# Optimization experiments

Hardware: AMD Instinct MI355X
Metric: run time of the kernel (lower is better)

Reference implementation:

```python
import jax, jax.numpy as jnp
import numpy as np

D_MODEL = 1024
N_HEADS = 16
D_HEAD = 64
D_REC = N_HEADS * D_HEAD  # 1024
BATCH = 4
SEQ = 8192
CHUNK = 64


def _make_decay_bias():
    n_fast, n_medium, n_slow = 5, 6, 5
    b = np.zeros(D_REC, dtype=np.float32)
    fast_end = n_fast * D_HEAD
    medium_end = (n_fast + n_medium) * D_HEAD
    b[:fast_end] = -2.2
    b[fast_end:medium_end] = 0.0
    b[medium_end:] = 4.6
    return jnp.asarray(b)


def setup_inputs() -> dict:
    key = jax.random.key(0)
    k_x, k_w1, k_w2 = jax.random.split(key, 3)
    x = jax.random.normal(k_x, (BATCH, SEQ, D_MODEL), dtype=jnp.float32)
    # nn.Linear(d_model, 3*d_rec, bias=False); stored as [in, out] for clean matmul
    W_aiv = jax.random.normal(k_w1, (D_MODEL, 3 * D_REC), dtype=jnp.float32) / np.sqrt(D_MODEL)
    decay_bias = _make_decay_bias()
    W_mix = jax.random.normal(k_w2, (D_REC, D_MODEL), dtype=jnp.float32) / np.sqrt(D_REC)
    b_mix = jnp.zeros((D_MODEL,), dtype=jnp.float32)
    return {"x": x, "W_aiv": W_aiv, "decay_bias": decay_bias, "W_mix": W_mix, "b_mix": b_mix}


def _chunked_scan(decay, value, chunk_size=CHUNK):
    # decay, value: [b, s, d] float32; gated linear recurrence h_t = a_t*h_{t-1} + u_t
    b, s, d = decay.shape
    pad = (-s) % chunk_size
    if pad:
        decay = jnp.pad(decay, ((0, 0), (0, pad), (0, 0)), constant_values=1.0)
        value = jnp.pad(value, ((0, 0), (0, pad), (0, 0)))
    total = s + pad
    n = total // chunk_size
    dc = decay.reshape(b, n, chunk_size, d)
    vc = value.reshape(b, n, chunk_size, d)
    # intra-chunk: cumulative decay products in log space
    cum_log = jnp.cumsum(jnp.log(jnp.maximum(dc, 1e-10)), axis=2)
    cum_decay = jnp.exp(cum_log)
    weighted = vc / jnp.maximum(cum_decay, 1e-10)
    intra_state = cum_decay * jnp.cumsum(weighted, axis=2)
    # cross-chunk propagation
    chunk_final_state = intra_state[:, :, -1, :]   # [b, n, d]
    chunk_total_decay = cum_decay[:, :, -1, :]     # [b, n, d]
    cum_log_chunk = jnp.cumsum(jnp.log(jnp.maximum(chunk_total_decay, 1e-10)), axis=1)
    cum_chunk_decay = jnp.exp(cum_log_chunk)
    cum_weighted_chunk = jnp.cumsum(chunk_final_state / jnp.maximum(cum_chunk_decay, 1e-10), axis=1)
    zeros = jnp.zeros((b, 1, d), dtype=cum_weighted_chunk.dtype)
    ones = jnp.ones((b, 1, d), dtype=cum_chunk_decay.dtype)
    incoming_cum_weighted = jnp.concatenate([zeros, cum_weighted_chunk[:, :-1]], axis=1)
    incoming_cum_decay = jnp.concatenate([ones, cum_chunk_decay[:, :-1]], axis=1)
    incoming_state = incoming_cum_decay * incoming_cum_weighted  # [b, n, d]
    cross_contrib = cum_decay * incoming_state[:, :, None, :]
    states = (intra_state + cross_contrib).reshape(b, total, d)[:, :s]
    return states


def reference(x, W_aiv, decay_bias, W_mix, b_mix):
    aiv = x @ W_aiv  # [b, s, 3*d_rec]
    a_proj, i_proj, v = jnp.split(aiv, 3, axis=-1)
    a = jax.nn.sigmoid(a_proj + decay_bias)
    i = jax.nn.sigmoid(i_proj)
    input_signal = jnp.sqrt(jnp.maximum(1.0 - a * a, 1e-8)) * (i * v)
    h = _chunked_scan(a.astype(jnp.float32), input_signal.astype(jnp.float32))
    h = h.astype(x.dtype)
    return h @ W_mix + b_mix
```

## Files before the change

### kernel.cpp

```cpp
#include <hip/hip_runtime.h>
#include <cstdint>
#include <cstddef>

#define BATCH   4
#define SEQ     8192
#define DREC    1024
#define CHUNK   64
#define NCHUNK  128
#define M_TOT   (BATCH*SEQ)
#define N_AIV   3072

#define BM 256
#define BN 256
#define BK 32
#define NBUF 4

typedef _Float16 half8 __attribute__((ext_vector_type(8)));
typedef _Float16 half4 __attribute__((ext_vector_type(4)));
typedef float   floatx4 __attribute__((ext_vector_type(4)));

#define LOG2E   1.4426950408889634f
#define NLOG2EPS 33.219281f


__device__ __forceinline__ void gl_lds16(const void* g, void* l) {
    __builtin_amdgcn_global_load_lds(
        (const __attribute__((address_space(1))) void*)g,
        (__attribute__((address_space(3))) void*)l, 16, 0, 0);
}

__device__ __forceinline__ float fast_sigmoid(float z) {
    float e = __builtin_amdgcn_exp2f(-LOG2E * z);
    return __builtin_amdgcn_rcpf(1.f + e);
}

template <bool F16_OUT, bool TWO_PHASE>
__global__ __launch_bounds__(512, 2) void gemm_ff(
    const _Float16* __restrict__ A, int lda,
    const _Float16* __restrict__ BT, int ldb,
    void* __restrict__ Cv, int ldc, int K,
    const float* __restrict__ bias)
{
    __shared__ __align__(16) _Float16 sm[NBUF * 16384];

    const int tid  = threadIdx.x;
    const int lane = tid & 63;
    const int wave = tid >> 6;

    const int nwg = gridDim.x * gridDim.y;
    int lin = blockIdx.y * gridDim.x + blockIdx.x;
    {
        const int cpx = nwg >> 3;
        lin = (lin & 7) * cpx + (lin >> 3);
    }
    const int bx = lin % gridDim.x;
    const int by = lin / gridDim.x;
    const int bm = by * BM;
    const int bn = bx * BN;
    const int wm = (wave >> 2) * 128;
    const int wn = (wave & 3) * 64;

    floatx4 acc[8][4];
    const floatx4 z4 = {0.f, 0.f, 0.f, 0.f};
    #pragma unroll
    for (int i = 0; i < 8; ++i)
        #pragma unroll
        for (int j = 0; j < 4; ++j) acc[i][j] = z4;

    const int o0 = tid * 16, o1 = o0 + 8192;
    const int r0 = o0 >> 6, s0 = (o0 >> 4) & 3;
    const int r1 = o1 >> 6, s1 = (o1 >> 4) & 3;
    const int g0 = (s0 ^ ((r0 >> 1) & 3)) * 8;
    const int g1 = (s1 ^ ((r1 >> 1) & 3)) * 8;
    const size_t aRow0 = (size_t)(bm + r0) * lda;
    const size_t aRow1 = (size_t)(bm + r1) * lda;
    const size_t bRow0 = (size_t)(bn + r0) * ldb;
    const size_t bRow1 = (size_t)(bn + r1) * ldb;

    auto stageA = [&](int t) {
        const int k0 = t * BK;
        char* base = (char*)sm + (t & (NBUF - 1)) * 32768;
        gl_lds16(A + aRow0 + k0 + g0, base + o0);
        gl_lds16(A + aRow1 + k0 + g1, base + o1);
    };
    auto stageB = [&](int t) {
        const int k0 = t * BK;
        char* base = (char*)sm + (t & (NBUF - 1)) * 32768;
        gl_lds16(BT + bRow0 + k0 + g0, base + 16384 + o0);
        gl_lds16(BT + bRow1 + k0 + g1, base + 16384 + o1);
    };

    const int fm = lane & 15;
    const int fq = lane >> 4;
    const int m0 = wm + fm;
    const int n0 = wn + fm;
    const int aoff0 = m0 * BK + ((fq ^ ((m0 >> 1) & 3)) << 3);
    const int boff0 = n0 * BK + ((fq ^ ((n0 >> 1) & 3)) << 3);

    const int NT = K / BK;
    stageA(0); stageB(0);
    if (NT > 1) { stageA(1); stageB(1); }
    if (NT > 2) { stageA(2); stageB(2); }

    for (int t = 0; t < NT; ++t) {
        const int rem = NT - 1 - t;
        if (rem >= 2)      asm volatile("s_waitcnt vmcnt(8)" ::: "memory");
        else if (rem == 1) asm volatile("s_waitcnt vmcnt(4)" ::: "memory");
        else               asm volatile("s_waitcnt vmcnt(0)" ::: "memory");
        __builtin_amdgcn_s_barrier();
        __builtin_amdgcn_sched_barrier(0);

        const _Float16* sA = sm + (t & (NBUF - 1)) * 16384;
        const _Float16* sB = sA + 8192;

        if constexpr (!TWO_PHASE) {
            if (t + 3 < NT) { stageA(t + 3); stageB(t + 3); }

            half8 ah[8], bh[4];
            #pragma unroll
            for (int i = 0; i < 8; ++i) ah[i] = *(const half8*)&sA[aoff0 + i * 16 * BK];
            #pragma unroll
            for (int j = 0; j < 4; ++j) bh[j] = *(const half8*)&sB[boff0 + j * 16 * BK];

            __builtin_amdgcn_s_setprio(1);
            #pragma unroll
            for (int i = 0; i < 8; ++i)
                #pragma unroll
                for (int j = 0; j < 4; ++j)
                    acc[i][j] = __builtin_amdgcn_mfma_f32_16x16x32_f16(
                        ah[i], bh[j], acc[i][j], 0, 0, 0);
            __builtin_amdgcn_s_setprio(0);
            __builtin_amdgcn_sched_barrier(0);
        } else {
            half8 ah[8], bh01[2];
            #pragma unroll
            for (int i = 0; i < 8; ++i) ah[i] = *(const half8*)&sA[aoff0 + i * 16 * BK];
            bh01[0] = *(const half8*)&sB[boff0 + 0 * 16 * BK];
            bh01[1] = *(const half8*)&sB[boff0 + 1 * 16 * BK];
            if (t + 3 < NT) stageA(t + 3);
            __builtin_amdgcn_s_barrier();
            asm volatile("s_waitcnt lgkmcnt(0)" ::: "memory");
            __builtin_amdgcn_sched_barrier(0);

            half8 bh23[2];
            bh23[0] = *(const half8*)&sB[boff0 + 2 * 16 * BK];
            bh23[1] = *(const half8*)&sB[boff0 + 3 * 16 * BK];

            __builtin_amdgcn_s_setprio(1);
            #pragma unroll
            for (int i = 0; i < 8; ++i) {
                acc[i][0] = __builtin_amdgcn_mfma_f32_16x16x32_f16(ah[i], bh01[0], acc[i][0], 0, 0, 0);
                acc[i][1] = __builtin_amdgcn_mfma_f32_16x16x32_f16(ah[i], bh01[1], acc[i][1], 0, 0, 0);
            }
            __builtin_amdgcn_s_setprio(0);
            __builtin_amdgcn_sched_barrier(0);

            if (t + 3 < NT) stageB(t + 3);
            __builtin_amdgcn_s_barrier();
            asm volatile("s_waitcnt lgkmcnt(0)" ::: "memory");
            __builtin_amdgcn_sched_barrier(0);

            __builtin_amdgcn_s_setprio(1);
            #pragma unroll
            for (int i = 0; i < 8; ++i) {
                acc[i][2] = __builtin_amdgcn_mfma_f32_16x16x32_f16(ah[i], bh23[0], acc[i][2], 0, 0, 0);
                acc[i][3] = __builtin_amdgcn_mfma_f32_16x16x32_f16(ah[i], bh23[1], acc[i][3], 0, 0, 0);
            }
            __builtin_amdgcn_s_setprio(0);
            __builtin_amdgcn_sched_barrier(0);
        }
    }

    const int er = (lane >> 4) * 4;
    const int ec = lane & 15;
    #pragma unroll
    for (int j = 0; j < 4; ++j) {
        int col = bn + wn + j * 16 + ec;
        float bj = (!F16_OUT && bias) ? bias[col] : 0.f;
        #pragma unroll
        for (int i = 0; i < 8; ++i) {
            int rowb = bm + wm + i * 16 + er;
            #pragma unroll
            for (int r = 0; r < 4; ++r) {
                if (F16_OUT)
                    ((_Float16*)Cv)[(size_t)(rowb + r) * ldc + col] =
                        (_Float16)acc[i][j][r];
                else
                    ((float*)Cv)[(size_t)(rowb + r) * ldc + col] =
                        acc[i][j][r] + bj;
            }
        }
    }
}

__global__ __launch_bounds__(256) void cvt_to_f16(
    const float* __restrict__ src, _Float16* __restrict__ dst)
{
    const size_t stride = (size_t)gridDim.x * 256 * 8;
    size_t i = ((size_t)blockIdx.x * 256 + threadIdx.x) * 8;
    #pragma unroll 2
    for (; i < (size_t)M_TOT * DREC; i += stride) {
        float4 a = *(const float4*)(src + i);
        float4 b = *(const float4*)(src + i + 4);
        half8 h;
        h[0] = (_Float16)a.x; h[1] = (_Float16)a.y;
        h[2] = (_Float16)a.z; h[3] = (_Float16)a.w;
        h[4] = (_Float16)b.x; h[5] = (_Float16)b.y;
        h[6] = (_Float16)b.z; h[7] = (_Float16)b.w;
        *(half8*)(dst + i) = h;
    }
}

__global__ __launch_bounds__(256) void transpose_cvt(
    const float* __restrict__ W, int K, int N, _Float16* __restrict__ T)
{
    __shared__ float tile[32][33];
    const int k0 = blockIdx.y * 32, n0 = blockIdx.x * 32;
    const int tx = threadIdx.x & 31, ty = threadIdx.x >> 5;
    #pragma unroll
    for (int r = 0; r < 32; r += 8)
        tile[ty + r][tx] = W[(size_t)(k0 + ty + r) * N + n0 + tx];
    __syncthreads();
    #pragma unroll
    for (int r = 0; r < 32; r += 8)
        T[(size_t)(n0 + ty + r) * K + k0 + tx] = (_Float16)tile[tx][ty + r];
}

__global__ __launch_bounds__(256) void scan_chunks(
    const _Float16* __restrict__ aivh, const float* __restrict__ decay_bias,
    float* __restrict__ ctd, float* __restrict__ cfs)
{
    int g  = blockIdx.x * 256 + threadIdx.x;
    int d4 = g & 255;
    int bc = g >> 8;

    const _Float16* base =
        aivh + ((size_t)bc * CHUNK) * 3072 + (size_t)d4 * 4;
    float4 db4 = *(const float4*)&decay_bias[d4 * 4];
    float db[4] = {db4.x, db4.y, db4.z, db4.w};

    float cl2[4] = {0, 0, 0, 0}, cw[4] = {0, 0, 0, 0};

    auto step = [&](half4 ap, half4 ip, half4 vv) {
        #pragma unroll
        for (int e = 0; e < 4; ++e) {
            float a  = fast_sigmoid((float)ap[e] + db[e]);
            float ii = fast_sigmoid((float)ip[e]);
            float s  = __builtin_amdgcn_sqrtf(fmaxf(1.f - a * a, 1e-8f))
                       * (ii * (float)vv[e]);
            cl2[e] += __builtin_amdgcn_logf(fmaxf(a, 1e-10f));
            float inv = __builtin_amdgcn_exp2f(fminf(-cl2[e], NLOG2EPS));
            cw[e] += s * inv;
        }
    };

    half4 as[8], ps[8], vs[8];
    #pragma unroll
    for (int j = 0; j < 8; ++j) {
        const _Float16* q = base + (size_t)j * 3072;
        as[j] = *(const half4*)q;
        ps[j] = *(const half4*)(q + 1024);
        vs[j] = *(const half4*)(q + 2048);
    }
    for (int k = 0; k < 8; ++k) {
        #pragma unroll
        for (int j = 0; j < 8; ++j) {
            step(as[j], ps[j], vs[j]);
            int nr = k * 8 + 8 + j;
            if (nr < CHUNK) {
                const _Float16* q = base + (size_t)nr * 3072;
                as[j] = *(const half4*)q;
                ps[j] = *(const half4*)(q + 1024);
                vs[j] = *(const half4*)(q + 2048);
            }
        }
    }

    float cd[4];
    #pragma unroll
    for (int e = 0; e < 4; ++e) cd[e] = __builtin_amdgcn_exp2f(cl2[e]);

    size_t so = (size_t)bc * 1024 + (size_t)d4 * 4;
    *(float4*)&ctd[so] = make_float4(cd[0], cd[1], cd[2], cd[3]);
    *(float4*)&cfs[so] = make_float4(cd[0] * cw[0], cd[1] * cw[1],
                                     cd[2] * cw[2], cd[3] * cw[3]);
}

__global__ __launch_bounds__(64) void scan_inter(
    const float* __restrict__ ctd, const float* __restrict__ cfs,
    float* __restrict__ incoming)
{
    int g = blockIdx.x * 64 + threadIdx.x;
    int d = g & 1023;
    int b = g >> 10;

    const size_t base = (size_t)b * NCHUNK * 1024 + (size_t)d;
    float cum2 = 0.f, cwc = 0.f;
    float pccd = 1.f, pcwc = 0.f;

    float t0 = ctd[base], f0 = cfs[base];
    float t1 = ctd[base + 1024], f1 = cfs[base + 1024];
    for (int n = 0; n < NCHUNK - 2; n += 2) {
        float t2 = ctd[base + (size_t)(n + 2) * 1024];
        float f2 = cfs[base + (size_t)(n + 2) * 1024];
        float t3 = ctd[base + (size_t)(n + 3) * 1024];
        float f3 = cfs[base + (size_t)(n + 3) * 1024];

        incoming[base + (size_t)n * 1024] = (n == 0) ? 0.f : pccd * pcwc;
        cum2 += __builtin_amdgcn_logf(fmaxf(t0, 1e-10f));
        float ccd = __builtin_amdgcn_exp2f(cum2);
        cwc += f0 * __builtin_amdgcn_exp2f(fminf(-cum2, NLOG2EPS));
        pccd = ccd; pcwc = cwc;

        incoming[base + (size_t)(n + 1) * 1024] = pccd * pcwc;
        cum2 += __builtin_amdgcn_logf(fmaxf(t1, 1e-10f));
        ccd = __builtin_amdgcn_exp2f(cum2);
        cwc += f1 * __builtin_amdgcn_exp2f(fminf(-cum2, NLOG2EPS));
        pccd = ccd; pcwc = cwc;

        t0 = t2; f0 = f2; t1 = t3; f1 = f3;
    }
    incoming[base + (size_t)(NCHUNK - 2) * 1024] = pccd * pcwc;
    cum2 += __builtin_amdgcn_logf(fmaxf(t0, 1e-10f));
    pccd = __builtin_amdgcn_exp2f(cum2);
    cwc += f0 * __builtin_amdgcn_exp2f(fminf(-cum2, NLOG2EPS));
    pcwc = cwc;
    incoming[base + (size_t)(NCHUNK - 1) * 1024] = pccd * pcwc;
}

__global__ __launch_bounds__(256) void scan_apply(
    const _Float16* __restrict__ aivh, const float* __restrict__ decay_bias,
    const float* __restrict__ incoming, _Float16* __restrict__ hb)
{
    int g  = blockIdx.x * 256 + threadIdx.x;
    int d4 = g & 255;
    int bc = g >> 8;

    const _Float16* base =
        aivh + ((size_t)bc * CHUNK) * 3072 + (size_t)d4 * 4;
    _Float16* hbase = hb + ((size_t)bc * CHUNK) * 1024 + (size_t)d4 * 4;
    float4 db4 = *(const float4*)&decay_bias[d4 * 4];
    float db[4] = {db4.x, db4.y, db4.z, db4.w};
    float4 ic4 = *(const float4*)&incoming[(size_t)bc * 1024 + d4 * 4];
    float inc[4] = {ic4.x, ic4.y, ic4.z, ic4.w};

    float cl2[4] = {0, 0, 0, 0}, cw[4] = {0, 0, 0, 0};

    auto step = [&](half4 ap, half4 ip, half4 vv, int row) {
        half4 h;
        #pragma unroll
        for (int e = 0; e < 4; ++e) {
            float a  = fast_sigmoid((float)ap[e] + db[e]);
            float ii = fast_sigmoid((float)ip[e]);
            float s  = __builtin_amdgcn_sqrtf(fmaxf(1.f - a * a, 1e-8f))
                       * (ii * (float)vv[e]);
            cl2[e] += __builtin_amdgcn_logf(fmaxf(a, 1e-10f));
            float inv = __builtin_amdgcn_exp2f(fminf(-cl2[e], NLOG2EPS));
            cw[e] += s * inv;
            float cd = __builtin_amdgcn_exp2f(cl2[e]);
            h[e] = (_Float16)(cd * (cw[e] + inc[e]));
        }
        *(half4*)&hbase[(size_t)row * 1024] = h;
    };

    half4 as[8], ps[8], vs[8];
    #pragma unroll
    for (int j = 0; j < 8; ++j) {
        const _Float16* q = base + (size_t)j * 3072;
        as[j] = *(const half4*)q;
        ps[j] = *(const half4*)(q + 1024);
        vs[j] = *(const half4*)(q + 2048);
    }
    for (int k = 0; k < 8; ++k) {
        #pragma unroll
        for (int j = 0; j < 8; ++j) {
            step(as[j], ps[j], vs[j], k * 8 + j);
            int nr = k * 8 + 8 + j;
            if (nr < CHUNK) {
                const _Float16* q = base + (size_t)nr * 3072;
                as[j] = *(const half4*)q;
                ps[j] = *(const half4*)(q + 1024);
                vs[j] = *(const half4*)(q + 2048);
            }
        }
    }
}

extern "C" void kernel_launch(void* const* d_in, const int* in_sizes, int n_in,
                              void* d_out, int out_size, void* d_ws, size_t ws_size,
                              hipStream_t stream)
{
    const float* x          = (const float*)d_in[0];
    const float* W_aiv      = (const float*)d_in[1];
    const float* decay_bias = (const float*)d_in[2];
    const float* W_mix      = (const float*)d_in[3];
    const float* b_mix      = (const float*)d_in[4];
    float* out = (float*)d_out;

    _Float16* aivh  = (_Float16*)d_ws;
    _Float16* xh    = aivh + (size_t)M_TOT * N_AIV;
    float* ctd      = (float*)(xh + (size_t)M_TOT * DREC);
    float* cfs      = ctd + (size_t)BATCH * NCHUNK * DREC;
    float* incoming = cfs + (size_t)BATCH * NCHUNK * DREC;
    _Float16* wT    = (_Float16*)(incoming + (size_t)BATCH * NCHUNK * DREC);
    _Float16* mT    = wT + (size_t)N_AIV * DREC;
    _Float16* hb    = xh;

    cvt_to_f16<<<2048, 256, 0, stream>>>(x, xh);
    {
        dim3 g1(N_AIV / 32, DREC / 32);
        transpose_cvt<<<g1, 256, 0, stream>>>(W_aiv, DREC, N_AIV, wT);
        dim3 g2(DREC / 32, DREC / 32);
        transpose_cvt<<<g2, 256, 0, stream>>>(W_mix, DREC, DREC, mT);
    }
    {
        dim3 grid(N_AIV / BN, M_TOT / BM);
        gemm_ff<true, false><<<grid, 512, 0, stream>>>(xh, DREC, wT, DREC,
                                                       aivh, N_AIV, DREC, nullptr);
    }
    scan_chunks<<<(BATCH * NCHUNK * 256) / 256, 256, 0, stream>>>(
        aivh, decay_bias, ctd, cfs);
    scan_inter<<<(BATCH * DREC) / 64, 64, 0, stream>>>(ctd, cfs, incoming);
    scan_apply<<<(BATCH * NCHUNK * 256) / 256, 256, 0, stream>>>(
        aivh, decay_bias, incoming, hb);
    {
        dim3 grid(DREC / BN, M_TOT / BM);
        gemm_ff<false, true><<<grid, 512, 0, stream>>>(hb, DREC, mT, DREC,
                                                       out, DREC, DREC, b_mix);
    }
}
```

Baseline: 659.4 us.

## Restructure GEMM mainloop to BK=64 double buffer with quartered LDS-read/MFMA phases

The fp16 GEMM changes from a 4-deep pipeline of BK=32 tiles to a 2-deep pipeline of BK=64 tiles, using an 8-way XOR swizzle for the 128-byte rows. Each K-step is split into four sub-phases that load half of the A or B fragments from LDS and then issue MFMAs, with barriers between them. Each iteration now issues the next global-to-LDS stage at its end. The intent is fewer barriers per unit of K, larger MFMA batches and less register pressure, at the cost of a shallower prefetch depth and more intra-iteration barriers.

```diff
diff --git a/kernel.cpp b/kernel.cpp
--- a/kernel.cpp
+++ b/kernel.cpp
@@ -12,8 +12,7 @@
 
 #define BM 256
 #define BN 256
-#define BK 32
-#define NBUF 4
+#define BK 64
 
 typedef _Float16 half8 __attribute__((ext_vector_type(8)));
 typedef _Float16 half4 __attribute__((ext_vector_type(4)));
@@ -34,14 +33,14 @@
     return __builtin_amdgcn_rcpf(1.f + e);
 }
 
-template <bool F16_OUT, bool TWO_PHASE>
+template <bool F16_OUT>
 __global__ __launch_bounds__(512, 2) void gemm_ff(
     const _Float16* __restrict__ A, int lda,
     const _Float16* __restrict__ BT, int ldb,
     void* __restrict__ Cv, int ldc, int K,
     const float* __restrict__ bias)
 {
-    __shared__ __align__(16) _Float16 sm[NBUF * 16384];
+    __shared__ __align__(16) _Float16 sm[2 * 32768];
 
     const int tid  = threadIdx.x;
     const int lane = tid & 63;
@@ -67,108 +66,87 @@
         #pragma unroll
         for (int j = 0; j < 4; ++j) acc[i][j] = z4;
 
-    const int o0 = tid * 16, o1 = o0 + 8192;
-    const int r0 = o0 >> 6, s0 = (o0 >> 4) & 3;
-    const int r1 = o1 >> 6, s1 = (o1 >> 4) & 3;
-    const int g0 = (s0 ^ ((r0 >> 1) & 3)) * 8;
-    const int g1 = (s1 ^ ((r1 >> 1) & 3)) * 8;
-    const size_t aRow0 = (size_t)(bm + r0) * lda;
-    const size_t aRow1 = (size_t)(bm + r1) * lda;
-    const size_t bRow0 = (size_t)(bn + r0) * ldb;
-    const size_t bRow1 = (size_t)(bn + r1) * ldb;
-
-    auto stageA = [&](int t) {
+    const int rS   = tid >> 3;
+    const int esrc = (((tid & 7) ^ ((tid >> 3) & 7)) << 3);
+
+    auto stage = [&](int t) {
         const int k0 = t * BK;
-        char* base = (char*)sm + (t & (NBUF - 1)) * 32768;
-        gl_lds16(A + aRow0 + k0 + g0, base + o0);
-        gl_lds16(A + aRow1 + k0 + g1, base + o1);
-    };
-    auto stageB = [&](int t) {
-        const int k0 = t * BK;
-        char* base = (char*)sm + (t & (NBUF - 1)) * 32768;
-        gl_lds16(BT + bRow0 + k0 + g0, base + 16384 + o0);
-        gl_lds16(BT + bRow1 + k0 + g1, base + 16384 + o1);
+        char* base = (char*)sm + (t & 1) * 65536;
+        #pragma unroll
+        for (int c = 0; c < 4; ++c)
+            gl_lds16(A + (size_t)(bm + rS + c * 64) * lda + k0 + esrc,
+                     base + tid * 16 + c * 8192);
+        #pragma unroll
+        for (int c = 0; c < 4; ++c)
+            gl_lds16(BT + (size_t)(bn + rS + c * 64) * ldb + k0 + esrc,
+                     base + 32768 + tid * 16 + c * 8192);
     };
 
     const int fm = lane & 15;
     const int fq = lane >> 4;
     const int m0 = wm + fm;
     const int n0 = wn + fm;
-    const int aoff0 = m0 * BK + ((fq ^ ((m0 >> 1) & 3)) << 3);
-    const int boff0 = n0 * BK + ((fq ^ ((n0 >> 1) & 3)) << 3);
+    const int ka = ((fq ^ (fm & 7)) << 3);
+    const int kb = ka ^ 32;
 
     const int NT = K / BK;
-    stageA(0); stageB(0);
-    if (NT > 1) { stageA(1); stageB(1); }
-    if (NT > 2) { stageA(2); stageB(2); }
+    stage(0);
+    if (NT > 1) stage(1);
 
     for (int t = 0; t < NT; ++t) {
-        const int rem = NT - 1 - t;
-        if (rem >= 2)      asm volatile("s_waitcnt vmcnt(8)" ::: "memory");
-        else if (rem == 1) asm volatile("s_waitcnt vmcnt(4)" ::: "memory");
-        else               asm volatile("s_waitcnt vmcnt(0)" ::: "memory");
+        if (t < NT - 1) asm volatile("s_waitcnt vmcnt(8)" ::: "memory");
+        else            asm volatile("s_waitcnt vmcnt(0)" ::: "memory");
         __builtin_amdgcn_s_barrier();
         __builtin_amdgcn_sched_barrier(0);
 
-        const _Float16* sA = sm + (t & (NBUF - 1)) * 16384;
-        const _Float16* sB = sA + 8192;
-
-        if constexpr (!TWO_PHASE) {
-            if (t + 3 < NT) { stageA(t + 3); stageB(t + 3); }
-
-            half8 ah[8], bh[4];
+        const _Float16* sA = sm + (t & 1) * 32768;
+        const _Float16* sB = sA + 16384;
+
+        half8 ah[4][2], bh[2][2];
+
+        auto ldA = [&](int ihalf) {
             #pragma unroll
-            for (int i = 0; i < 8; ++i) ah[i] = *(const half8*)&sA[aoff0 + i * 16 * BK];
+            for (int ii = 0; ii < 4; ++ii) {
+                const int m = m0 + (ihalf * 4 + ii) * 16;
+                ah[ii][0] = *(const half8*)&sA[m * 64 + ka];
+                ah[ii][1] = *(const half8*)&sA[m * 64 + kb];
+            }
+        };
+        auto ldB = [&](int jhalf) {
             #pragma unroll
-            for (int j = 0; j < 4; ++j) bh[j] = *(const half8*)&sB[boff0 + j * 16 * BK];
-
-            __builtin_amdgcn_s_setprio(1);
-            #pragma unroll
-            for (int i = 0; i < 8; ++i)
-                #pragma unroll
-                for (int j = 0; j < 4; ++j)
-                    acc[i][j] = __builtin_amdgcn_mfma_f32_16x16x32_f16(
-                        ah[i], bh[j], acc[i][j], 0, 0, 0);
-            __builtin_amdgcn_s_setprio(0);
-            __builtin_amdgcn_sched_barrier(0);
-        } else {
-            half8 ah[8], bh01[2];
-            #pragma unroll
-            for (int i = 0; i < 8; ++i) ah[i] = *(const half8*)&sA[aoff0 + i * 16 * BK];
-            bh01[0] = *(const half8*)&sB[boff0 + 0 * 16 * BK];
-            bh01[1] = *(const half8*)&sB[boff0 + 1 * 16 * BK];
-            if (t + 3 < NT) stageA(t + 3);
+            for (int jj = 0; jj < 2; ++jj) {
+                const int n = n0 + (jhalf * 2 + jj) * 16;
+                bh[jj][0] = *(const half8*)&sB[n * 64 + ka];
+                bh[jj][1] = *(const half8*)&sB[n * 64 + kb];
+            }
+        };
+        auto sync = [&]() {
             __builtin_amdgcn_s_barrier();
             asm volatile("s_waitcnt lgkmcnt(0)" ::: "memory");
             __builtin_amdgcn_sched_barrier(0);
-
-            half8 bh23[2];
-            bh23[0] = *(const half8*)&sB[boff0 + 2 * 16 * BK];
-            bh23[1] = *(const half8*)&sB[boff0 + 3 * 16 * BK];
-
+        };
+        auto domfma = [&](int ihalf, int jhalf) {
             __builtin_amdgcn_s_setprio(1);
             #pragma unroll
-            for (int i = 0; i < 8; ++i) {
-                acc[i][0] = __builtin_amdgcn_mfma_f32_16x16x32_f16(ah[i], bh01[0], acc[i][0], 0, 0, 0);
-                acc[i][1] = __builtin_amdgcn_mfma_f32_16x16x32_f16(ah[i], bh01[1], acc[i][1], 0, 0, 0);
-            }
+            for (int ii = 0; ii < 4; ++ii)
+                #pragma unroll
+                for (int jj = 0; jj < 2; ++jj) {
+                    const int i = ihalf * 4 + ii, j = jhalf * 2 + jj;
+                    acc[i][j] = __builtin_amdgcn_mfma_f32_16x16x32_f16(
+                        ah[ii][0], bh[jj][0], acc[i][j], 0, 0, 0);
+                    acc[i][j] = __builtin_amdgcn_mfma_f32_16x16x32_f16(
+                        ah[ii][1], bh[jj][1], acc[i][j], 0, 0, 0);
+                }
             __builtin_amdgcn_s_setprio(0);
             __builtin_amdgcn_sched_barrier(0);
-
-            if (t + 3 < NT) stageB(t + 3);
-            __builtin_amdgcn_s_barrier();
-            asm volatile("s_waitcnt lgkmcnt(0)" ::: "memory");
-            __builtin_amdgcn_sched_barrier(0);
-
-            __builtin_amdgcn_s_setprio(1);
-            #pragma unroll
-            for (int i = 0; i < 8; ++i) {
-                acc[i][2] = __builtin_amdgcn_mfma_f32_16x16x32_f16(ah[i], bh23[0], acc[i][2], 0, 0, 0);
-                acc[i][3] = __builtin_amdgcn_mfma_f32_16x16x32_f16(ah[i], bh23[1], acc[i][3], 0, 0, 0);
-            }
-            __builtin_amdgcn_s_setprio(0);
-            __builtin_amdgcn_sched_barrier(0);
-        }
+        };
+
+        ldA(0); ldB(0); sync(); domfma(0, 0); __builtin_amdgcn_s_barrier();
+        ldB(1);         sync(); domfma(0, 1); __builtin_amdgcn_s_barrier();
+        ldA(1);         sync(); domfma(1, 1); __builtin_amdgcn_s_barrier();
+        ldB(0);         sync(); domfma(1, 0); __builtin_amdgcn_s_barrier();
+
+        if (t + 2 < NT) stage(t + 2);
     }
 
     const int er = (lane >> 4) * 4;
@@ -415,8 +393,8 @@
     }
     {
         dim3 grid(N_AIV / BN, M_TOT / BM);
-        gemm_ff<true, false><<<grid, 512, 0, stream>>>(xh, DREC, wT, DREC,
-                                                       aivh, N_AIV, DREC, nullptr);
+        gemm_ff<true><<<grid, 512, 0, stream>>>(xh, DREC, wT, DREC,
+                                                aivh, N_AIV, DREC, nullptr);
     }
     scan_chunks<<<(BATCH * NCHUNK * 256) / 256, 256, 0, stream>>>(
         aivh, decay_bias, ctd, cfs);
@@ -425,7 +403,7 @@
         aivh, decay_bias, incoming, hb);
     {
         dim3 grid(DREC / BN, M_TOT / BM);
-        gemm_ff<false, true><<<grid, 512, 0, stream>>>(hb, DREC, mT, DREC,
-                                                       out, DREC, DREC, b_mix);
-    }
-}
+        gemm_ff<false><<<grid, 512, 0, stream>>>(hb, DREC, mT, DREC,
+                                                 out, DREC, DREC, b_mix);
+    }
+}
```

Result: slower. 678.4 us (+2.9%).
